# Kernel optimization log

Measured on AMD Instinct MI355X. Metric: run time of the kernel, lower is better.

Reference implementation:

```python
import jax, jax.numpy as jnp
import numpy as np

N_EMB = 768
N_HEAD = 12
D_HEAD = N_EMB // N_HEAD


def setup_inputs() -> dict:
    key = jax.random.key(0)
    k0, k1, k2, k3, k4 = jax.random.split(key, 5)
    B, T = 2, 2048
    s = 1.0 / np.sqrt(N_EMB)
    return {
        "x": jax.random.normal(k0, (B, T, N_EMB), dtype=jnp.float32),
        "w_q": jax.random.normal(k1, (N_EMB, N_EMB), dtype=jnp.float32) * s,
        "w_k": jax.random.normal(k2, (N_EMB, N_EMB), dtype=jnp.float32) * s,
        "w_v": jax.random.normal(k3, (N_EMB, N_EMB), dtype=jnp.float32) * s,
        "w_o": jax.random.normal(k4, (N_EMB, N_EMB), dtype=jnp.float32) * s,
    }


def reference(x, w_q, w_k, w_v, w_o):
    B, T, C = x.shape
    # project and split heads: [B, H, T, Dh]
    def proj(w):
        return jnp.einsum('btc,dc->btd', x, w).reshape(B, T, N_HEAD, D_HEAD).transpose(0, 2, 1, 3)
    q, k, v = proj(w_q), proj(w_k), proj(w_v)
    scores = jnp.einsum('bhqd,bhkd->bhqk', q, k)  # [B, H, T, T]
    causal = jnp.tril(jnp.ones((T, T), dtype=bool))  # keep j <= i
    scores = jnp.where(causal, scores, -jnp.inf)
    weights = jax.nn.softmax(scores / np.sqrt(D_HEAD).astype(np.float32), axis=-1)
    # dropout p=0.0 -> identity
    out = jnp.einsum('bhqk,bhkd->bhqd', weights, v)  # [B, H, T, Dh]
    out = out.transpose(0, 2, 1, 3).reshape(B, T, C)
    final = jnp.einsum('btc,dc->btd', out, w_o)
    return (final, weights)
```

## Files before the change

kernel.cpp:

```cpp
#include <hip/hip_runtime.h>
#include <stdint.h>
#include <stddef.h>

#define T_SEQ 2048
#define NH    12
#define DH    64
#define NB    2
#define NEMB  768

using f32x4  = __attribute__((ext_vector_type(4))) float;
using bf16x8 = __attribute__((ext_vector_type(8))) short;

#define MFMA(a, b, c) __builtin_amdgcn_mfma_f32_16x16x32_bf16((a), (b), (c), 0, 0, 0)

__device__ __forceinline__ short f2bf(float f) {
    union { float f; uint32_t u; } v; v.f = f;
    uint32_t u = v.u + 0x7FFFu + ((v.u >> 16) & 1u);
    return (short)(u >> 16);
}

__global__ void cvt_kernel(const float* __restrict__ x,  const float* __restrict__ wq,
                           const float* __restrict__ wk, const float* __restrict__ wv,
                           const float* __restrict__ wo,
                           short* __restrict__ xb,  short* __restrict__ wqb,
                           short* __restrict__ wkb, short* __restrict__ wvb,
                           short* __restrict__ wob) {
    const float* src; short* dst; int n;
    switch (blockIdx.y) {
        case 0:  src = x;  dst = xb;  n = NB * T_SEQ * NEMB; break;
        case 1:  src = wq; dst = wqb; n = NEMB * NEMB; break;
        case 2:  src = wk; dst = wkb; n = NEMB * NEMB; break;
        case 3:  src = wv; dst = wvb; n = NEMB * NEMB; break;
        default: src = wo; dst = wob; n = NEMB * NEMB; break;
    }
    int n4 = n >> 2;
    for (int i = blockIdx.x * blockDim.x + threadIdx.x; i < n4; i += gridDim.x * blockDim.x) {
        float4 v = ((const float4*)src)[i];
        short4 o;
        o.x = f2bf(v.x); o.y = f2bf(v.y); o.z = f2bf(v.z); o.w = f2bf(v.w);
        ((short4*)dst)[i] = o;
    }
}

__global__ __launch_bounds__(256, 2) void qkv_gemm(
        const short* __restrict__ xb,  const short* __restrict__ wqb,
        const short* __restrict__ wkb, const short* __restrict__ wvb,
        short* __restrict__ Qh, short* __restrict__ Kh, short* __restrict__ Vt) {
    __shared__ short As[128 * 64];
    __shared__ short Bs[128 * 64];
    const int mode = blockIdx.z;
    const short* Wm = (mode == 0) ? wqb : (mode == 1) ? wkb : wvb;
    const int rowbase = blockIdx.x * 128;
    const int colbase = blockIdx.y * 128;
    const int tid = threadIdx.x;
    const int lane = tid & 63;
    const int wid = tid >> 6;
    const int wm = wid >> 1, wn = wid & 1;
    const int g = lane >> 4, c = lane & 15;

    const f32x4 z4 = {0.f, 0.f, 0.f, 0.f};
    f32x4 acc[4][4];
#pragma unroll
    for (int i = 0; i < 4; ++i)
#pragma unroll
        for (int j = 0; j < 4; ++j) acc[i][j] = z4;

    for (int kt = 0; kt < 12; ++kt) {
        __syncthreads();
#pragma unroll
        for (int p = 0; p < 4; ++p) {
            int lin = p * 256 + tid;
            int row = lin >> 3, kb = lin & 7;
            int sw = ((kb * 16) ^ ((row & 7) << 4)) >> 1;
            *(bf16x8*)&As[row * 64 + sw] = *(const bf16x8*)&xb[(rowbase + row) * NEMB + kt * 64 + kb * 8];
            *(bf16x8*)&Bs[row * 64 + sw] = *(const bf16x8*)&Wm[(colbase + row) * NEMB + kt * 64 + kb * 8];
        }
        __syncthreads();
#pragma unroll
        for (int ks = 0; ks < 2; ++ks) {
            bf16x8 a[4], b[4];
#pragma unroll
            for (int mi = 0; mi < 4; ++mi) {
                int row = wm * 64 + mi * 16 + c;
                int kb = ((ks * 64 + g * 16) ^ ((row & 7) << 4)) >> 1;
                a[mi] = *(const bf16x8*)&As[row * 64 + kb];
            }
#pragma unroll
            for (int ni = 0; ni < 4; ++ni) {
                int row = wn * 64 + ni * 16 + c;
                int kb = ((ks * 64 + g * 16) ^ ((row & 7) << 4)) >> 1;
                b[ni] = *(const bf16x8*)&Bs[row * 64 + kb];
            }
#pragma unroll
            for (int mi = 0; mi < 4; ++mi)
#pragma unroll
                for (int ni = 0; ni < 4; ++ni)
                    acc[mi][ni] = MFMA(a[mi], b[ni], acc[mi][ni]);
        }
    }
#pragma unroll
    for (int mi = 0; mi < 4; ++mi) {
        int trow0 = rowbase + wm * 64 + mi * 16 + g * 4;
#pragma unroll
        for (int ni = 0; ni < 4; ++ni) {
            int col = colbase + wn * 64 + ni * 16 + c;
            int h = col >> 6, dh = col & 63;
#pragma unroll
            for (int r = 0; r < 4; ++r) {
                int trow = trow0 + r;
                int bb = trow >> 11, t = trow & 2047;
                int bh = bb * NH + h;
                short val = f2bf(acc[mi][ni][r]);
                if (mode == 2)      Vt[(size_t)bh * (DH * T_SEQ) + dh * T_SEQ + t] = val;
                else if (mode == 0) Qh[((size_t)bh * T_SEQ + t) * DH + dh] = val;
                else                Kh[((size_t)bh * T_SEQ + t) * DH + dh] = val;
            }
        }
    }
}

__global__ __launch_bounds__(256, 2) void attn_kernel(
        const short* __restrict__ Qh, const short* __restrict__ Kh,
        const short* __restrict__ Vt, float* __restrict__ Wout,
        short* __restrict__ Ob) {
    __shared__ short Ks[64 * 64];
    __shared__ short Vs[64 * 64];
    __shared__ short Ps[4][32 * 64];

    const int bh = blockIdx.y;
    const int bb = bh / NH, h = bh % NH;
    const int qtile = blockIdx.x;
    const int qbase = qtile * 128;
    const int tid = threadIdx.x, lane = tid & 63, w = tid >> 6;
    const int g = lane >> 4, c = lane & 15;
    const int nkt = 2 * (qtile + 1);
    const int stripmax = qbase + w * 32 + 31;

    const short* Qp = Qh + (size_t)bh * T_SEQ * DH;
    const short* Kp = Kh + (size_t)bh * T_SEQ * DH;
    const short* Vp = Vt + (size_t)bh * DH * T_SEQ;
    float* Wp = Wout + (size_t)bh * T_SEQ * T_SEQ;

    const f32x4 z4 = {0.f, 0.f, 0.f, 0.f};

    bf16x8 q[2][2];
#pragma unroll
    for (int mi = 0; mi < 2; ++mi)
#pragma unroll
        for (int ks = 0; ks < 2; ++ks)
            q[mi][ks] = *(const bf16x8*)&Qp[(qbase + w * 32 + mi * 16 + c) * DH + ks * 32 + g * 8];

    float lsum[2][4];
#pragma unroll
    for (int mi = 0; mi < 2; ++mi)
#pragma unroll
        for (int r = 0; r < 4; ++r) lsum[mi][r] = 0.f;

    for (int kt = 0; kt < nkt; ++kt) {
        __syncthreads();
#pragma unroll
        for (int p = 0; p < 2; ++p) {
            int lin = p * 256 + tid;
            int row = lin >> 3, kb = lin & 7;
            int sw = ((kb * 16) ^ ((row & 7) << 4)) >> 1;
            *(bf16x8*)&Ks[row * 64 + sw] = *(const bf16x8*)&Kp[(kt * 64 + row) * DH + kb * 8];
        }
        __syncthreads();
        if (kt * 64 > stripmax) continue;
#pragma unroll
        for (int ni = 0; ni < 4; ++ni) {
            f32x4 s[2] = {z4, z4};
#pragma unroll
            for (int ks = 0; ks < 2; ++ks) {
                int krow = ni * 16 + c;
                int kb = ((ks * 64 + g * 16) ^ ((krow & 7) << 4)) >> 1;
                bf16x8 kf = *(const bf16x8*)&Ks[krow * 64 + kb];
                s[0] = MFMA(q[0][ks], kf, s[0]);
                s[1] = MFMA(q[1][ks], kf, s[1]);
            }
            int colg = kt * 64 + ni * 16 + c;
#pragma unroll
            for (int mi = 0; mi < 2; ++mi) {
                int row0 = qbase + w * 32 + mi * 16 + g * 4;
#pragma unroll
                for (int r = 0; r < 4; ++r) {
                    float e = __expf(s[mi][r] * 0.125f);
                    lsum[mi][r] += (colg <= row0 + r) ? e : 0.f;
                }
            }
        }
    }
    float rl[2][4];
#pragma unroll
    for (int mi = 0; mi < 2; ++mi)
#pragma unroll
        for (int r = 0; r < 4; ++r) {
            float v = lsum[mi][r];
            v += __shfl_xor(v, 1); v += __shfl_xor(v, 2);
            v += __shfl_xor(v, 4); v += __shfl_xor(v, 8);
            rl[mi][r] = 1.0f / v;
        }

    f32x4 o[2][4];
#pragma unroll
    for (int mi = 0; mi < 2; ++mi)
#pragma unroll
        for (int di = 0; di < 4; ++di) o[mi][di] = z4;

    for (int kt = 0; kt < nkt; ++kt) {
        __syncthreads();
#pragma unroll
        for (int p = 0; p < 2; ++p) {
            int lin = p * 256 + tid;
            int row = lin >> 3, kb = lin & 7;
            int sw = ((kb * 16) ^ ((row & 7) << 4)) >> 1;
            *(bf16x8*)&Ks[row * 64 + sw] = *(const bf16x8*)&Kp[(kt * 64 + row) * DH + kb * 8];
            *(bf16x8*)&Vs[row * 64 + sw] = *(const bf16x8*)&Vp[row * T_SEQ + kt * 64 + kb * 8];
        }
        __syncthreads();
        if (kt * 64 > stripmax) {
            float4 z = make_float4(0.f, 0.f, 0.f, 0.f);
#pragma unroll
            for (int i = 0; i < 8; ++i) {
                int rowg = qbase + w * 32 + i * 4 + g;
                *(float4*)&Wp[(size_t)rowg * T_SEQ + kt * 64 + c * 4] = z;
            }
            continue;
        }
#pragma unroll
        for (int ni = 0; ni < 4; ++ni) {
            f32x4 s[2] = {z4, z4};
#pragma unroll
            for (int ks = 0; ks < 2; ++ks) {
                int krow = ni * 16 + c;
                int kb = ((ks * 64 + g * 16) ^ ((krow & 7) << 4)) >> 1;
                bf16x8 kf = *(const bf16x8*)&Ks[krow * 64 + kb];
                s[0] = MFMA(q[0][ks], kf, s[0]);
                s[1] = MFMA(q[1][ks], kf, s[1]);
            }
            int colg = kt * 64 + ni * 16 + c;
#pragma unroll
            for (int mi = 0; mi < 2; ++mi) {
                int rowl = w * 32 + mi * 16 + g * 4;
                float* wptr = Wp + (size_t)(qbase + rowl) * T_SEQ + colg;
#pragma unroll
                for (int r = 0; r < 4; ++r) {
                    float e = __expf(s[mi][r] * 0.125f);
                    float wgt = (colg <= qbase + rowl + r) ? e * rl[mi][r] : 0.f;
                    wptr[(size_t)r * T_SEQ] = wgt;
                    int prow = mi * 16 + g * 4 + r;
                    int pidx = prow * 64 + ((((ni * 16 + c) * 2) ^ ((prow & 7) << 4)) >> 1);
                    Ps[w][pidx] = f2bf(wgt);
                }
            }
        }
#pragma unroll
        for (int ks = 0; ks < 2; ++ks) {
            bf16x8 pa[2];
#pragma unroll
            for (int mi = 0; mi < 2; ++mi) {
                int prow = mi * 16 + c;
                int kb = ((ks * 64 + g * 16) ^ ((prow & 7) << 4)) >> 1;
                pa[mi] = *(const bf16x8*)&Ps[w][prow * 64 + kb];
            }
#pragma unroll
            for (int di = 0; di < 4; ++di) {
                int vrow = di * 16 + c;
                int kb = ((ks * 64 + g * 16) ^ ((vrow & 7) << 4)) >> 1;
                bf16x8 vf = *(const bf16x8*)&Vs[vrow * 64 + kb];
                o[0][di] = MFMA(pa[0], vf, o[0][di]);
                o[1][di] = MFMA(pa[1], vf, o[1][di]);
            }
        }
    }

    int c0 = nkt * 64;
    if (c0 < T_SEQ) {
        float4 z = make_float4(0.f, 0.f, 0.f, 0.f);
        for (int r = 0; r < 128; ++r) {
            size_t base = (size_t)(qbase + r) * T_SEQ;
            for (int cc = c0 + tid * 4; cc < T_SEQ; cc += 1024)
                *(float4*)&Wp[base + cc] = z;
        }
    }

#pragma unroll
    for (int mi = 0; mi < 2; ++mi)
#pragma unroll
        for (int di = 0; di < 4; ++di)
#pragma unroll
            for (int r = 0; r < 4; ++r) {
                int rowg = qbase + w * 32 + mi * 16 + g * 4 + r;
                Ob[(size_t)(bb * T_SEQ + rowg) * NEMB + h * 64 + di * 16 + c] = f2bf(o[mi][di][r]);
            }
}

__global__ __launch_bounds__(256, 2) void out_gemm(
        const short* __restrict__ Ob, const short* __restrict__ wob,
        float* __restrict__ outp) {
    __shared__ short As[128 * 64];
    __shared__ short Bs[128 * 64];
    const int rowbase = blockIdx.x * 128;
    const int colbase = blockIdx.y * 128;
    const int tid = threadIdx.x;
    const int lane = tid & 63;
    const int wid = tid >> 6;
    const int wm = wid >> 1, wn = wid & 1;
    const int g = lane >> 4, c = lane & 15;

    const f32x4 z4 = {0.f, 0.f, 0.f, 0.f};
    f32x4 acc[4][4];
#pragma unroll
    for (int i = 0; i < 4; ++i)
#pragma unroll
        for (int j = 0; j < 4; ++j) acc[i][j] = z4;

    for (int kt = 0; kt < 12; ++kt) {
        __syncthreads();
#pragma unroll
        for (int p = 0; p < 4; ++p) {
            int lin = p * 256 + tid;
            int row = lin >> 3, kb = lin & 7;
            int sw = ((kb * 16) ^ ((row & 7) << 4)) >> 1;
            *(bf16x8*)&As[row * 64 + sw] = *(const bf16x8*)&Ob[(rowbase + row) * NEMB + kt * 64 + kb * 8];
            *(bf16x8*)&Bs[row * 64 + sw] = *(const bf16x8*)&wob[(colbase + row) * NEMB + kt * 64 + kb * 8];
        }
        __syncthreads();
#pragma unroll
        for (int ks = 0; ks < 2; ++ks) {
            bf16x8 a[4], b[4];
#pragma unroll
            for (int mi = 0; mi < 4; ++mi) {
                int row = wm * 64 + mi * 16 + c;
                int kb = ((ks * 64 + g * 16) ^ ((row & 7) << 4)) >> 1;
                a[mi] = *(const bf16x8*)&As[row * 64 + kb];
            }
#pragma unroll
            for (int ni = 0; ni < 4; ++ni) {
                int row = wn * 64 + ni * 16 + c;
                int kb = ((ks * 64 + g * 16) ^ ((row & 7) << 4)) >> 1;
                b[ni] = *(const bf16x8*)&Bs[row * 64 + kb];
            }
#pragma unroll
            for (int mi = 0; mi < 4; ++mi)
#pragma unroll
                for (int ni = 0; ni < 4; ++ni)
                    acc[mi][ni] = MFMA(a[mi], b[ni], acc[mi][ni]);
        }
    }
#pragma unroll
    for (int mi = 0; mi < 4; ++mi) {
        int trow0 = rowbase + wm * 64 + mi * 16 + g * 4;
#pragma unroll
        for (int ni = 0; ni < 4; ++ni) {
            int col = colbase + wn * 64 + ni * 16 + c;
#pragma unroll
            for (int r = 0; r < 4; ++r)
                outp[(size_t)(trow0 + r) * NEMB + col] = acc[mi][ni][r];
        }
    }
}

extern "C" void kernel_launch(void* const* d_in, const int* in_sizes, int n_in,
                              void* d_out, int out_size, void* d_ws, size_t ws_size,
                              hipStream_t stream) {
    (void)in_sizes; (void)n_in; (void)out_size; (void)ws_size;
    const float* x  = (const float*)d_in[0];
    const float* wq = (const float*)d_in[1];
    const float* wk = (const float*)d_in[2];
    const float* wv = (const float*)d_in[3];
    const float* wo = (const float*)d_in[4];
    float* outp = (float*)d_out;
    float* wout = outp + (size_t)NB * T_SEQ * NEMB;

    char* ws = (char*)d_ws;
    size_t off = 0;
    short* xb  = (short*)(ws + off); off += (size_t)NB * T_SEQ * NEMB * 2;
    short* wqb = (short*)(ws + off); off += (size_t)NEMB * NEMB * 2;
    short* wkb = (short*)(ws + off); off += (size_t)NEMB * NEMB * 2;
    short* wvb = (short*)(ws + off); off += (size_t)NEMB * NEMB * 2;
    short* wob = (short*)(ws + off); off += (size_t)NEMB * NEMB * 2;
    short* Qh  = (short*)(ws + off); off += (size_t)NB * NH * T_SEQ * DH * 2;
    short* Kh  = (short*)(ws + off); off += (size_t)NB * NH * T_SEQ * DH * 2;
    short* Vt  = (short*)(ws + off); off += (size_t)NB * NH * T_SEQ * DH * 2;
    short* Ob  = (short*)(ws + off); off += (size_t)NB * T_SEQ * NEMB * 2;

    cvt_kernel<<<dim3(512, 5), 256, 0, stream>>>(x, wq, wk, wv, wo, xb, wqb, wkb, wvb, wob);
    qkv_gemm<<<dim3(32, 6, 3), 256, 0, stream>>>(xb, wqb, wkb, wvb, Qh, Kh, Vt);
    attn_kernel<<<dim3(16, NB * NH), 256, 0, stream>>>(Qh, Kh, Vt, wout, Ob);
    out_gemm<<<dim3(32, 6), 256, 0, stream>>>(Ob, wob, outp);
}
```

Before: 549.3 us.

## Transpose score MFMA layout and emit coalesced nontemporal weight stores from LDS

Swaps MFMA operands so each lane holds a query row, reducing the row-sum reduction to two shuffles. Folds the 1/sqrt(d)·log2e scale into the Q weight conversion and uses native exp2 and rcp. Softmax weights are now packed as bf16 into the shared P tile and re-read to issue wide coalesced nontemporal fp32 stores instead of scattered scalar stores. The trade-off is that the weights output now carries bf16 precision rather than fp32.

Result: slower. 575.3 us (+4.7%).

```diff
diff --git a/kernel.cpp b/kernel.cpp
--- a/kernel.cpp
+++ b/kernel.cpp
@@ -10,13 +10,20 @@
 
 using f32x4  = __attribute__((ext_vector_type(4))) float;
 using bf16x8 = __attribute__((ext_vector_type(8))) short;
+using bf16x4 = __attribute__((ext_vector_type(4))) short;
 
 #define MFMA(a, b, c) __builtin_amdgcn_mfma_f32_16x16x32_bf16((a), (b), (c), 0, 0, 0)
+
+extern "C" __device__ float __ocml_native_exp2_f32(float);
 
 __device__ __forceinline__ short f2bf(float f) {
     union { float f; uint32_t u; } v; v.f = f;
     uint32_t u = v.u + 0x7FFFu + ((v.u >> 16) & 1u);
     return (short)(u >> 16);
+}
+__device__ __forceinline__ float b2f(short s) {
+    union { uint32_t u; float f; } v; v.u = ((uint32_t)(uint16_t)s) << 16;
+    return v.f;
 }
 
 __global__ void cvt_kernel(const float* __restrict__ x,  const float* __restrict__ wq,
@@ -25,10 +32,10 @@
                            short* __restrict__ xb,  short* __restrict__ wqb,
                            short* __restrict__ wkb, short* __restrict__ wvb,
                            short* __restrict__ wob) {
-    const float* src; short* dst; int n;
+    const float* src; short* dst; int n; float scale = 1.0f;
     switch (blockIdx.y) {
         case 0:  src = x;  dst = xb;  n = NB * T_SEQ * NEMB; break;
-        case 1:  src = wq; dst = wqb; n = NEMB * NEMB; break;
+        case 1:  src = wq; dst = wqb; n = NEMB * NEMB; scale = 0.18033688737f; break;
         case 2:  src = wk; dst = wkb; n = NEMB * NEMB; break;
         case 3:  src = wv; dst = wvb; n = NEMB * NEMB; break;
         default: src = wo; dst = wob; n = NEMB * NEMB; break;
@@ -37,7 +44,8 @@
     for (int i = blockIdx.x * blockDim.x + threadIdx.x; i < n4; i += gridDim.x * blockDim.x) {
         float4 v = ((const float4*)src)[i];
         short4 o;
-        o.x = f2bf(v.x); o.y = f2bf(v.y); o.z = f2bf(v.z); o.w = f2bf(v.w);
+        o.x = f2bf(v.x * scale); o.y = f2bf(v.y * scale);
+        o.z = f2bf(v.z * scale); o.w = f2bf(v.w * scale);
         ((short4*)dst)[i] = o;
     }
 }
@@ -150,12 +158,7 @@
         for (int ks = 0; ks < 2; ++ks)
             q[mi][ks] = *(const bf16x8*)&Qp[(qbase + w * 32 + mi * 16 + c) * DH + ks * 32 + g * 8];
 
-    float lsum[2][4];
-#pragma unroll
-    for (int mi = 0; mi < 2; ++mi)
-#pragma unroll
-        for (int r = 0; r < 4; ++r) lsum[mi][r] = 0.f;
-
+    float lsum[2] = {0.f, 0.f};
     for (int kt = 0; kt < nkt; ++kt) {
         __syncthreads();
 #pragma unroll
@@ -175,37 +178,38 @@
                 int krow = ni * 16 + c;
                 int kb = ((ks * 64 + g * 16) ^ ((krow & 7) << 4)) >> 1;
                 bf16x8 kf = *(const bf16x8*)&Ks[krow * 64 + kb];
-                s[0] = MFMA(q[0][ks], kf, s[0]);
-                s[1] = MFMA(q[1][ks], kf, s[1]);
-            }
-            int colg = kt * 64 + ni * 16 + c;
+                s[0] = MFMA(kf, q[0][ks], s[0]);
+                s[1] = MFMA(kf, q[1][ks], s[1]);
+            }
+            int bcol = kt * 64 + ni * 16 + g * 4;
 #pragma unroll
             for (int mi = 0; mi < 2; ++mi) {
-                int row0 = qbase + w * 32 + mi * 16 + g * 4;
+                int rowg = qbase + w * 32 + mi * 16 + c;
 #pragma unroll
                 for (int r = 0; r < 4; ++r) {
-                    float e = __expf(s[mi][r] * 0.125f);
-                    lsum[mi][r] += (colg <= row0 + r) ? e : 0.f;
+                    float e = __ocml_native_exp2_f32(s[mi][r]);
+                    lsum[mi] += (bcol + r <= rowg) ? e : 0.f;
                 }
             }
         }
     }
-    float rl[2][4];
+    float rl[2];
+#pragma unroll
+    for (int mi = 0; mi < 2; ++mi) {
+        float t = lsum[mi];
+        t += __shfl_xor(t, 16);
+        t += __shfl_xor(t, 32);
+        rl[mi] = __builtin_amdgcn_rcpf(t);
+    }
+
+    f32x4 o[2][4];
 #pragma unroll
     for (int mi = 0; mi < 2; ++mi)
 #pragma unroll
-        for (int r = 0; r < 4; ++r) {
-            float v = lsum[mi][r];
-            v += __shfl_xor(v, 1); v += __shfl_xor(v, 2);
-            v += __shfl_xor(v, 4); v += __shfl_xor(v, 8);
-            rl[mi][r] = 1.0f / v;
-        }
-
-    f32x4 o[2][4];
-#pragma unroll
-    for (int mi = 0; mi < 2; ++mi)
-#pragma unroll
         for (int di = 0; di < 4; ++di) o[mi][di] = z4;
+
+    const int wl8 = lane >> 3;
+    const int cl8 = lane & 7;
 
     for (int kt = 0; kt < nkt; ++kt) {
         __syncthreads();
@@ -219,11 +223,11 @@
         }
         __syncthreads();
         if (kt * 64 > stripmax) {
-            float4 z = make_float4(0.f, 0.f, 0.f, 0.f);
-#pragma unroll
-            for (int i = 0; i < 8; ++i) {
-                int rowg = qbase + w * 32 + i * 4 + g;
-                *(float4*)&Wp[(size_t)rowg * T_SEQ + kt * 64 + c * 4] = z;
+#pragma unroll
+            for (int it = 0; it < 4; ++it) {
+                float* dst = Wp + (size_t)(qbase + w * 32 + it * 8 + wl8) * T_SEQ + kt * 64 + cl8 * 8;
+                __builtin_nontemporal_store(z4, (f32x4*)dst);
+                __builtin_nontemporal_store(z4, (f32x4*)(dst + 4));
             }
             continue;
         }
@@ -235,23 +239,23 @@
                 int krow = ni * 16 + c;
                 int kb = ((ks * 64 + g * 16) ^ ((krow & 7) << 4)) >> 1;
                 bf16x8 kf = *(const bf16x8*)&Ks[krow * 64 + kb];
-                s[0] = MFMA(q[0][ks], kf, s[0]);
-                s[1] = MFMA(q[1][ks], kf, s[1]);
-            }
-            int colg = kt * 64 + ni * 16 + c;
+                s[0] = MFMA(kf, q[0][ks], s[0]);
+                s[1] = MFMA(kf, q[1][ks], s[1]);
+            }
+            int bcol = kt * 64 + ni * 16 + g * 4;
 #pragma unroll
             for (int mi = 0; mi < 2; ++mi) {
-                int rowl = w * 32 + mi * 16 + g * 4;
-                float* wptr = Wp + (size_t)(qbase + rowl) * T_SEQ + colg;
+                int rowg = qbase + w * 32 + mi * 16 + c;
+                bf16x4 pk;
 #pragma unroll
                 for (int r = 0; r < 4; ++r) {
-                    float e = __expf(s[mi][r] * 0.125f);
-                    float wgt = (colg <= qbase + rowl + r) ? e * rl[mi][r] : 0.f;
-                    wptr[(size_t)r * T_SEQ] = wgt;
-                    int prow = mi * 16 + g * 4 + r;
-                    int pidx = prow * 64 + ((((ni * 16 + c) * 2) ^ ((prow & 7) << 4)) >> 1);
-                    Ps[w][pidx] = f2bf(wgt);
+                    float e = __ocml_native_exp2_f32(s[mi][r]) * rl[mi];
+                    float wgt = (bcol + r <= rowg) ? e : 0.f;
+                    pk[r] = f2bf(wgt);
                 }
+                int prow = mi * 16 + c;
+                int sw = ((ni * 32 + g * 8) ^ ((prow & 7) << 4)) >> 1;
+                *(bf16x4*)&Ps[w][prow * 64 + sw] = pk;
             }
         }
 #pragma unroll
@@ -272,15 +276,25 @@
                 o[1][di] = MFMA(pa[1], vf, o[1][di]);
             }
         }
+#pragma unroll
+        for (int it = 0; it < 4; ++it) {
+            int prow = it * 8 + wl8;
+            int sw = ((cl8 * 16) ^ ((prow & 7) << 4)) >> 1;
+            bf16x8 pv8 = *(const bf16x8*)&Ps[w][prow * 64 + sw];
+            float* dst = Wp + (size_t)(qbase + w * 32 + prow) * T_SEQ + kt * 64 + cl8 * 8;
+            f32x4 lo = {b2f(pv8[0]), b2f(pv8[1]), b2f(pv8[2]), b2f(pv8[3])};
+            f32x4 hi = {b2f(pv8[4]), b2f(pv8[5]), b2f(pv8[6]), b2f(pv8[7])};
+            __builtin_nontemporal_store(lo, (f32x4*)dst);
+            __builtin_nontemporal_store(hi, (f32x4*)(dst + 4));
+        }
     }
 
     int c0 = nkt * 64;
     if (c0 < T_SEQ) {
-        float4 z = make_float4(0.f, 0.f, 0.f, 0.f);
         for (int r = 0; r < 128; ++r) {
-            size_t base = (size_t)(qbase + r) * T_SEQ;
+            float* base = Wp + (size_t)(qbase + r) * T_SEQ;
             for (int cc = c0 + tid * 4; cc < T_SEQ; cc += 1024)
-                *(float4*)&Wp[base + cc] = z;
+                __builtin_nontemporal_store(z4, (f32x4*)(base + cc));
         }
     }
 
```
